# Performance work log

Hardware: AMD Instinct MI355X
Metric: run time of the kernel (lower is better)

## Reference

```python
import jax, jax.numpy as jnp
import numpy as np

K = 10          # top-k history news selected per candidate
THRESHOLD = 0.1 # attention-weight threshold (config.threshold)
EPS = 1e-12     # F.normalize eps


def setup_inputs() -> dict:
    key = jax.random.key(0)
    k1, k2, k3, k4 = jax.random.split(key, 4)
    B, C, H, L, LEV, D = 32, 5, 50, 32, 3, 256
    return {
        "cdd_repr": jax.random.normal(k1, (B, C, D), dtype=jnp.float32),
        "his_repr": jax.random.normal(k2, (B, H, D), dtype=jnp.float32),
        "his_embedding": jax.random.normal(k3, (B, H, L, LEV, D), dtype=jnp.float32),
        "W_sel": jax.random.normal(k4, (D, D), dtype=jnp.float32) * (1.0 / np.sqrt(D)),
        "b_sel": jnp.zeros((D,), dtype=jnp.float32),
    }


def _l2norm(x):
    # F.normalize(x, dim=-1): x / max(||x||, eps)
    n = jnp.sqrt(jnp.sum(x * x, axis=-1, keepdims=True))
    return x / jnp.maximum(n, EPS)


def reference(cdd_repr, his_repr, his_embedding, W_sel, b_sel):
    # selectionProject (Linear) + L2 normalize
    c = _l2norm(cdd_repr @ W_sel + b_sel)      # [B, C, D]
    h = _l2norm(his_repr @ W_sel + b_sel)      # [B, H, D]
    # news-level attention scores: cdd x his
    attn = jnp.einsum('bcd,bhd->bch', c, h)    # [B, C, H]
    # top-k over history
    w, idx = jax.lax.top_k(attn, K)            # [B, C, K]
    # gather selected history embeddings: [B, C, K, L, LEV, D]
    B = his_embedding.shape[0]
    his_activated = his_embedding[jnp.arange(B)[:, None, None], idx]
    # threshold masking then scale activated embeddings by attention weight
    w_masked = jnp.where(w < THRESHOLD, 0.0, w)
    his_activated = his_activated * w_masked[:, :, :, None, None, None]
    return his_activated
```

## Files before the change

### kernel.cpp

```cpp
#include <hip/hip_runtime.h>
#include <math.h>

#define BB 32
#define CC 5
#define HH 50
#define LL 32
#define LEV 3
#define DD 256
#define KK 10
#define THRESH 0.1f
#define EPSF 1e-12f
#define RPB 8
#define NROWS (BB * CC + BB * HH)

typedef float f32x4 __attribute__((ext_vector_type(4)));

__global__ void proj_norm_kernel(const float* __restrict__ cdd,
                                 const float* __restrict__ his,
                                 const float* __restrict__ W,
                                 const float* __restrict__ bias,
                                 float* __restrict__ c_out,
                                 float* __restrict__ h_out)
{
    const int row0 = blockIdx.x * RPB;
    const int j    = threadIdx.x;
    const int wid  = j >> 6;
    const int lane = j & 63;

    __shared__ float xs[RPB][DD];
    #pragma unroll
    for (int r = 0; r < RPB; ++r) {
        const int row = row0 + r;
        const float* x = (row < BB * CC) ? (cdd + (size_t)row * DD)
                                         : (his + (size_t)(row - BB * CC) * DD);
        xs[r][j] = x[j];
    }
    __syncthreads();

    const float bj = bias[j];
    float acc[RPB];
    #pragma unroll
    for (int r = 0; r < RPB; ++r) acc[r] = bj;

    for (int d = 0; d < DD; d += 4) {
        const float w0 = W[(size_t)(d + 0) * DD + j];
        const float w1 = W[(size_t)(d + 1) * DD + j];
        const float w2 = W[(size_t)(d + 2) * DD + j];
        const float w3 = W[(size_t)(d + 3) * DD + j];
        #pragma unroll
        for (int r = 0; r < RPB; ++r) {
            const float4 xv = *(const float4*)&xs[r][d];
            acc[r] = fmaf(xv.x, w0, fmaf(xv.y, w1, fmaf(xv.z, w2, fmaf(xv.w, w3, acc[r]))));
        }
    }

    __shared__ float part[RPB][4];
    #pragma unroll
    for (int r = 0; r < RPB; ++r) {
        float s = acc[r] * acc[r];
        #pragma unroll
        for (int off = 32; off > 0; off >>= 1) s += __shfl_xor(s, off, 64);
        if (lane == 0) part[r][wid] = s;
    }
    __syncthreads();
    __shared__ float inv_s[RPB];
    if (j < RPB) {
        const float s = part[j][0] + part[j][1] + part[j][2] + part[j][3];
        inv_s[j] = 1.0f / fmaxf(sqrtf(s), EPSF);
    }
    __syncthreads();

    #pragma unroll
    for (int r = 0; r < RPB; ++r) {
        const int row = row0 + r;
        float* y = (row < BB * CC) ? (c_out + (size_t)row * DD)
                                   : (h_out + (size_t)(row - BB * CC) * DD);
        y[j] = acc[r] * inv_s[r];
    }
}

__global__ void attn_topk_kernel(const float* __restrict__ c_n,
                                 const float* __restrict__ h_n,
                                 float* __restrict__ w_out,
                                 int* __restrict__ idx_out)
{
    const int bc   = blockIdx.x;
    const int b    = bc / CC;
    const int tid  = threadIdx.x;
    const int wid  = tid >> 6;
    const int lane = tid & 63;

    __shared__ float cs[DD];
    __shared__ float attn_s[64];
    cs[tid] = c_n[(size_t)bc * DD + tid];
    if (tid < 64) attn_s[tid] = -INFINITY;
    __syncthreads();

    for (int h = wid; h < HH; h += 4) {
        const float* hr = h_n + (size_t)(b * HH + h) * DD;
        float p = 0.f;
        #pragma unroll
        for (int i = 0; i < 4; ++i) p += cs[lane + i * 64] * hr[lane + i * 64];
        #pragma unroll
        for (int off = 32; off > 0; off >>= 1) p += __shfl_down(p, off, 64);
        if (lane == 0) attn_s[h] = p;
    }
    __syncthreads();

    if (wid == 0) {
        float v   = attn_s[lane];
        int   myi = lane;
        for (int k = 0; k < KK; ++k) {
            float bv = v;
            int   bi = myi;
            #pragma unroll
            for (int off = 32; off > 0; off >>= 1) {
                const float ov = __shfl_xor(bv, off, 64);
                const int   oi = __shfl_xor(bi, off, 64);
                if (ov > bv || (ov == bv && oi < bi)) { bv = ov; bi = oi; }
            }
            if (lane == 0) {
                w_out[bc * KK + k]   = (bv < THRESH) ? 0.0f : bv;
                idx_out[bc * KK + k] = bi;
            }
            if (myi == bi) v = -INFINITY;
        }
    }
}

#define CHUNKS 4
__global__ void gather_scale_kernel(const float* __restrict__ emb,
                                    const float* __restrict__ w,
                                    const int* __restrict__ idx,
                                    float* __restrict__ out)
{
    const int INNER  = LL * LEV * DD;
    const int INNER4 = INNER / 4;
    const int PER    = INNER4 / CHUNKS;

    const int g     = blockIdx.x;
    const int blk   = g / CHUNKS;
    const int chunk = g % CHUNKS;
    const int b     = blk / (CC * KK);

    const float wv = w[blk];
    const int   hi = idx[blk];

    f32x4* dst = (f32x4*)(out + (size_t)blk * INNER) + (size_t)chunk * PER;

    if (wv == 0.0f) {
        const f32x4 z = (f32x4){0.f, 0.f, 0.f, 0.f};
        for (int i = threadIdx.x; i < PER; i += 256)
            __builtin_nontemporal_store(z, &dst[i]);
    } else {
        const f32x4* src = (const f32x4*)(emb + (size_t)(b * HH + hi) * INNER)
                           + (size_t)chunk * PER;
        for (int i = threadIdx.x; i < PER; i += 256) {
            const f32x4 v = src[i];
            __builtin_nontemporal_store(v * wv, &dst[i]);
        }
    }
}

extern "C" void kernel_launch(void* const* d_in, const int* in_sizes, int n_in,
                              void* d_out, int out_size, void* d_ws, size_t ws_size,
                              hipStream_t stream) {
    const float* cdd  = (const float*)d_in[0];
    const float* his  = (const float*)d_in[1];
    const float* emb  = (const float*)d_in[2];
    const float* W    = (const float*)d_in[3];
    const float* bias = (const float*)d_in[4];
    float* out = (float*)d_out;

    char* ws = (char*)d_ws;
    float* c_n = (float*)ws;
    float* h_n = (float*)(ws + 163840);
    float* wv  = (float*)(ws + 163840 + 1638400);
    int*   idx = (int*)  (ws + 163840 + 1638400 + 6400);

    proj_norm_kernel<<<NROWS / RPB, DD, 0, stream>>>(cdd, his, W, bias, c_n, h_n);
    attn_topk_kernel<<<BB * CC, DD, 0, stream>>>(c_n, h_n, wv, idx);
    gather_scale_kernel<<<BB * CC * KK * CHUNKS, 256, 0, stream>>>(emb, wv, idx, out);
}
```

Measured before the change: 78.29 us.

## Fuse projection, top-k and gather into one cooperative persistent kernel

Replaces three kernel launches with a single cooperative kernel of 512 blocks that runs the projection, the attention top-k and the gather-scale stages separated by grid-wide syncs. The gather stage becomes a grid-stride loop with fully unrolled accesses, and its nontemporal stores are replaced by plain stores. This removes launch gaps and inter-kernel drain. In exchange it adds grid.sync overhead, limits the gather stage to 512 blocks, and may cost write bandwidth without nontemporal stores.

```diff
diff --git a/kernel.cpp b/kernel.cpp
--- a/kernel.cpp
+++ b/kernel.cpp
@@ -1,5 +1,8 @@
 #include <hip/hip_runtime.h>
+#include <hip/hip_cooperative_groups.h>
 #include <math.h>
+
+namespace cg = cooperative_groups;
 
 #define BB 32
 #define CC 5
@@ -11,153 +14,156 @@
 #define THRESH 0.1f
 #define EPSF 1e-12f
 #define RPB 8
-#define NROWS (BB * CC + BB * HH)
+#define NPROJ 220
+#define NBLK 512
+#define INNER (LL * LEV * DD)
+#define INNER4 (INNER / 4)
+#define CHUNKS 4
+#define PERCH (INNER4 / CHUNKS)
+#define NCHUNK (BB * CC * KK * CHUNKS)
 
 typedef float f32x4 __attribute__((ext_vector_type(4)));
 
-__global__ void proj_norm_kernel(const float* __restrict__ cdd,
-                                 const float* __restrict__ his,
-                                 const float* __restrict__ W,
-                                 const float* __restrict__ bias,
-                                 float* __restrict__ c_out,
-                                 float* __restrict__ h_out)
+__global__ __launch_bounds__(256, 4)
+void fused_kernel(const float* __restrict__ cdd,
+                  const float* __restrict__ his,
+                  const float* __restrict__ emb,
+                  const float* __restrict__ W,
+                  const float* __restrict__ bias,
+                  float* __restrict__ c_n,
+                  float* __restrict__ h_n,
+                  float* __restrict__ wv,
+                  int* __restrict__ idx,
+                  float* __restrict__ out)
 {
-    const int row0 = blockIdx.x * RPB;
+    cg::grid_group grid = cg::this_grid();
+    const int bid  = blockIdx.x;
     const int j    = threadIdx.x;
     const int wid  = j >> 6;
     const int lane = j & 63;
 
-    __shared__ float xs[RPB][DD];
-    #pragma unroll
-    for (int r = 0; r < RPB; ++r) {
-        const int row = row0 + r;
-        const float* x = (row < BB * CC) ? (cdd + (size_t)row * DD)
-                                         : (his + (size_t)(row - BB * CC) * DD);
-        xs[r][j] = x[j];
-    }
-    __syncthreads();
+    if (bid < NPROJ) {
+        const int row0 = bid * RPB;
 
-    const float bj = bias[j];
-    float acc[RPB];
-    #pragma unroll
-    for (int r = 0; r < RPB; ++r) acc[r] = bj;
-
-    for (int d = 0; d < DD; d += 4) {
-        const float w0 = W[(size_t)(d + 0) * DD + j];
-        const float w1 = W[(size_t)(d + 1) * DD + j];
-        const float w2 = W[(size_t)(d + 2) * DD + j];
-        const float w3 = W[(size_t)(d + 3) * DD + j];
+        __shared__ float xs[RPB][DD];
         #pragma unroll
         for (int r = 0; r < RPB; ++r) {
-            const float4 xv = *(const float4*)&xs[r][d];
-            acc[r] = fmaf(xv.x, w0, fmaf(xv.y, w1, fmaf(xv.z, w2, fmaf(xv.w, w3, acc[r]))));
+            const int row = row0 + r;
+            const float* x = (row < BB * CC) ? (cdd + (size_t)row * DD)
+                                             : (his + (size_t)(row - BB * CC) * DD);
+            xs[r][j] = x[j];
+        }
+        __syncthreads();
+
+        const float bj = bias[j];
+        float acc[RPB];
+        #pragma unroll
+        for (int r = 0; r < RPB; ++r) acc[r] = bj;
+
+        for (int d = 0; d < DD; d += 4) {
+            const float w0 = W[(size_t)(d + 0) * DD + j];
+            const float w1 = W[(size_t)(d + 1) * DD + j];
+            const float w2 = W[(size_t)(d + 2) * DD + j];
+            const float w3 = W[(size_t)(d + 3) * DD + j];
+            #pragma unroll
+            for (int r = 0; r < RPB; ++r) {
+                const float4 xv = *(const float4*)&xs[r][d];
+                acc[r] = fmaf(xv.x, w0, fmaf(xv.y, w1, fmaf(xv.z, w2, fmaf(xv.w, w3, acc[r]))));
+            }
+        }
+
+        __shared__ float part[RPB][4];
+        #pragma unroll
+        for (int r = 0; r < RPB; ++r) {
+            float s = acc[r] * acc[r];
+            #pragma unroll
+            for (int off = 32; off > 0; off >>= 1) s += __shfl_xor(s, off, 64);
+            if (lane == 0) part[r][wid] = s;
+        }
+        __syncthreads();
+        __shared__ float inv_s[RPB];
+        if (j < RPB) {
+            const float s = part[j][0] + part[j][1] + part[j][2] + part[j][3];
+            inv_s[j] = 1.0f / fmaxf(sqrtf(s), EPSF);
+        }
+        __syncthreads();
+
+        #pragma unroll
+        for (int r = 0; r < RPB; ++r) {
+            const int row = row0 + r;
+            float* y = (row < BB * CC) ? (c_n + (size_t)row * DD)
+                                       : (h_n + (size_t)(row - BB * CC) * DD);
+            y[j] = acc[r] * inv_s[r];
         }
     }
 
-    __shared__ float part[RPB][4];
-    #pragma unroll
-    for (int r = 0; r < RPB; ++r) {
-        float s = acc[r] * acc[r];
-        #pragma unroll
-        for (int off = 32; off > 0; off >>= 1) s += __shfl_xor(s, off, 64);
-        if (lane == 0) part[r][wid] = s;
-    }
-    __syncthreads();
-    __shared__ float inv_s[RPB];
-    if (j < RPB) {
-        const float s = part[j][0] + part[j][1] + part[j][2] + part[j][3];
-        inv_s[j] = 1.0f / fmaxf(sqrtf(s), EPSF);
-    }
-    __syncthreads();
+    grid.sync();
 
-    #pragma unroll
-    for (int r = 0; r < RPB; ++r) {
-        const int row = row0 + r;
-        float* y = (row < BB * CC) ? (c_out + (size_t)row * DD)
-                                   : (h_out + (size_t)(row - BB * CC) * DD);
-        y[j] = acc[r] * inv_s[r];
-    }
-}
+    if (bid < BB * CC) {
+        const int bc = bid;
+        const int b  = bc / CC;
 
-__global__ void attn_topk_kernel(const float* __restrict__ c_n,
-                                 const float* __restrict__ h_n,
-                                 float* __restrict__ w_out,
-                                 int* __restrict__ idx_out)
-{
-    const int bc   = blockIdx.x;
-    const int b    = bc / CC;
-    const int tid  = threadIdx.x;
-    const int wid  = tid >> 6;
-    const int lane = tid & 63;
+        __shared__ float cs[DD];
+        __shared__ float attn_s[64];
+        cs[j] = c_n[(size_t)bc * DD + j];
+        if (j < 64) attn_s[j] = -INFINITY;
+        __syncthreads();
 
-    __shared__ float cs[DD];
-    __shared__ float attn_s[64];
-    cs[tid] = c_n[(size_t)bc * DD + tid];
-    if (tid < 64) attn_s[tid] = -INFINITY;
-    __syncthreads();
+        for (int h = wid; h < HH; h += 4) {
+            const float* hr = h_n + (size_t)(b * HH + h) * DD;
+            float p = 0.f;
+            #pragma unroll
+            for (int i = 0; i < 4; ++i) p += cs[lane + i * 64] * hr[lane + i * 64];
+            #pragma unroll
+            for (int off = 32; off > 0; off >>= 1) p += __shfl_down(p, off, 64);
+            if (lane == 0) attn_s[h] = p;
+        }
+        __syncthreads();
 
-    for (int h = wid; h < HH; h += 4) {
-        const float* hr = h_n + (size_t)(b * HH + h) * DD;
-        float p = 0.f;
-        #pragma unroll
-        for (int i = 0; i < 4; ++i) p += cs[lane + i * 64] * hr[lane + i * 64];
-        #pragma unroll
-        for (int off = 32; off > 0; off >>= 1) p += __shfl_down(p, off, 64);
-        if (lane == 0) attn_s[h] = p;
-    }
-    __syncthreads();
-
-    if (wid == 0) {
-        float v   = attn_s[lane];
-        int   myi = lane;
-        for (int k = 0; k < KK; ++k) {
-            float bv = v;
-            int   bi = myi;
-            #pragma unroll
-            for (int off = 32; off > 0; off >>= 1) {
-                const float ov = __shfl_xor(bv, off, 64);
-                const int   oi = __shfl_xor(bi, off, 64);
-                if (ov > bv || (ov == bv && oi < bi)) { bv = ov; bi = oi; }
+        if (wid == 0) {
+            float v   = attn_s[lane];
+            int   myi = lane;
+            for (int k = 0; k < KK; ++k) {
+                float bv = v;
+                int   bi = myi;
+                #pragma unroll
+                for (int off = 32; off > 0; off >>= 1) {
+                    const float ov = __shfl_xor(bv, off, 64);
+                    const int   oi = __shfl_xor(bi, off, 64);
+                    if (ov > bv || (ov == bv && oi < bi)) { bv = ov; bi = oi; }
+                }
+                if (lane == 0) {
+                    wv[bc * KK + k]  = (bv < THRESH) ? 0.0f : bv;
+                    idx[bc * KK + k] = bi;
+                }
+                if (myi == bi) v = -INFINITY;
             }
-            if (lane == 0) {
-                w_out[bc * KK + k]   = (bv < THRESH) ? 0.0f : bv;
-                idx_out[bc * KK + k] = bi;
-            }
-            if (myi == bi) v = -INFINITY;
         }
     }
-}
 
-#define CHUNKS 4
-__global__ void gather_scale_kernel(const float* __restrict__ emb,
-                                    const float* __restrict__ w,
-                                    const int* __restrict__ idx,
-                                    float* __restrict__ out)
-{
-    const int INNER  = LL * LEV * DD;
-    const int INNER4 = INNER / 4;
-    const int PER    = INNER4 / CHUNKS;
+    grid.sync();
 
-    const int g     = blockIdx.x;
-    const int blk   = g / CHUNKS;
-    const int chunk = g % CHUNKS;
-    const int b     = blk / (CC * KK);
+    for (int g = bid; g < NCHUNK; g += NBLK) {
+        const int blk   = g >> 2;
+        const int chunk = g & 3;
+        const int b     = blk / (CC * KK);
 
-    const float wv = w[blk];
-    const int   hi = idx[blk];
+        const float w_ = wv[blk];
+        const int   hi = idx[blk];
 
-    f32x4* dst = (f32x4*)(out + (size_t)blk * INNER) + (size_t)chunk * PER;
+        f32x4* dst = (f32x4*)(out + (size_t)blk * INNER) + (size_t)chunk * PERCH;
 
-    if (wv == 0.0f) {
-        const f32x4 z = (f32x4){0.f, 0.f, 0.f, 0.f};
-        for (int i = threadIdx.x; i < PER; i += 256)
-            __builtin_nontemporal_store(z, &dst[i]);
-    } else {
-        const f32x4* src = (const f32x4*)(emb + (size_t)(b * HH + hi) * INNER)
-                           + (size_t)chunk * PER;
-        for (int i = threadIdx.x; i < PER; i += 256) {
-            const f32x4 v = src[i];
-            __builtin_nontemporal_store(v * wv, &dst[i]);
+        if (w_ == 0.0f) {
+            const f32x4 z = (f32x4){0.f, 0.f, 0.f, 0.f};
+            #pragma unroll
+            for (int u = 0; u < PERCH / 256; ++u)
+                dst[j + 256 * u] = z;
+        } else {
+            const f32x4* src = (const f32x4*)(emb + (size_t)(b * HH + hi) * INNER)
+                               + (size_t)chunk * PERCH;
+            #pragma unroll
+            for (int u = 0; u < PERCH / 256; ++u)
+                dst[j + 256 * u] = src[j + 256 * u] * w_;
         }
     }
 }
@@ -175,10 +181,11 @@
     char* ws = (char*)d_ws;
     float* c_n = (float*)ws;
     float* h_n = (float*)(ws + 163840);
-    float* wv  = (float*)(ws + 163840 + 1638400);
-    int*   idx = (int*)  (ws + 163840 + 1638400 + 6400);
+    float* wvp = (float*)(ws + 163840 + 1638400);
+    int*   idp = (int*)  (ws + 163840 + 1638400 + 6400);
 
-    proj_norm_kernel<<<NROWS / RPB, DD, 0, stream>>>(cdd, his, W, bias, c_n, h_n);
-    attn_topk_kernel<<<BB * CC, DD, 0, stream>>>(c_n, h_n, wv, idx);
-    gather_scale_kernel<<<BB * CC * KK * CHUNKS, 256, 0, stream>>>(emb, wv, idx, out);
+    void* args[] = { (void*)&cdd, (void*)&his, (void*)&emb, (void*)&W, (void*)&bias,
+                     (void*)&c_n, (void*)&h_n, (void*)&wvp, (void*)&idp, (void*)&out };
+    hipLaunchCooperativeKernel((const void*)fused_kernel,
+                               dim3(NBLK), dim3(256), args, 0, stream);
 }
```

After: 182.9 us. 2.34x slower.
